# Performance work log

Measured on AMD Instinct MI355X. Metric: run time of the kernel, lower is better.

The kernel has to match this reference:

```python
import jax, jax.numpy as jnp
import numpy as np

LATENT, HIDDEN, OUT = 128, 256, 8
T, B = 32, 16384
LN_EPS = 1e-5
SLOPE = 0.1  # LeakyReLU negative slope


def _leaky(x):
    return jnp.where(x >= 0, x, SLOPE * x)


def _mlp_layer(x, W, b, g, beta):
    # Linear -> LayerNorm -> LeakyReLU(0.1)
    h = x @ W + b
    mu = jnp.mean(h, axis=-1, keepdims=True)
    var = jnp.mean(jnp.square(h - mu), axis=-1, keepdims=True)
    h = (h - mu) * jax.lax.rsqrt(var + LN_EPS) * g + beta
    return _leaky(h)


def setup_inputs() -> dict:
    key = jax.random.key(0)
    ks = jax.random.split(key, 12)
    rn = lambda k, shape, s: jax.random.normal(k, shape, jnp.float32) * s
    z0 = rn(ks[0], (B, LATENT), 1.0)
    # strictly increasing per-sample timestamps [T, B, 1]
    dts = jax.random.uniform(ks[1], (T, B, 1), jnp.float32, 0.01, 0.1)
    ts = jnp.cumsum(dts, axis=0)
    W1 = rn(ks[2], (LATENT + 1, HIDDEN), (LATENT + 1) ** -0.5)
    b1 = jnp.zeros((HIDDEN,), jnp.float32)
    g1 = jnp.ones((HIDDEN,), jnp.float32)
    be1 = jnp.zeros((HIDDEN,), jnp.float32)
    W2 = rn(ks[3], (HIDDEN, LATENT), HIDDEN ** -0.5)
    b2 = jnp.zeros((LATENT,), jnp.float32)
    g2 = jnp.ones((LATENT,), jnp.float32)
    be2 = jnp.zeros((LATENT,), jnp.float32)
    Wl = rn(ks[4], (LATENT, HIDDEN), LATENT ** -0.5)
    bl = jnp.zeros((HIDDEN,), jnp.float32)
    Wo = rn(ks[5], (HIDDEN, OUT), HIDDEN ** -0.5)
    bo = jnp.zeros((OUT,), jnp.float32)
    return dict(z0=z0, ts=ts, W1=W1, b1=b1, g1=g1, be1=be1,
                W2=W2, b2=b2, g2=g2, be2=be2, Wl=Wl, bl=bl, Wo=Wo, bo=bo)


def reference(z0, ts, W1, b1, g1, be1, W2, b2, g2, be2, Wl, bl, Wo, bo):
    def f(z, t):  # MLPODEF: concat time, 2 (Linear->LN->LeakyReLU) layers
        zt = jnp.concatenate([z, t], axis=-1)           # [B, LATENT+1]
        h = _mlp_layer(zt, W1, b1, g1, be1)             # [B, HIDDEN]
        return _mlp_layer(h, W2, b2, g2, be2)           # [B, LATENT]

    t0 = jnp.zeros((1,) + ts.shape[1:], ts.dtype)
    ts_all = jnp.concatenate([t0, ts], axis=0)          # [T+1, B, 1]

    def rk4_step(z, tt):  # one fixed RK4 step per consecutive timestamp pair
        t_cur, t_next = tt                               # [B,1] each
        dt = t_next - t_cur
        k1 = f(z, t_cur)
        k2 = f(z + 0.5 * dt * k1, t_cur + 0.5 * dt)
        k3 = f(z + 0.5 * dt * k2, t_cur + 0.5 * dt)
        k4 = f(z + dt * k3, t_next)
        z_new = z + (dt / 6.0) * (k1 + 2.0 * k2 + 2.0 * k3 + k4)
        return z_new, z_new

    _, zs = jax.lax.scan(rk4_step, z0, (ts_all[:-1], ts_all[1:]))  # [T,B,LATENT] == zs[1:]
    hs = _leaky(zs @ Wl + bl)                            # [T,B,HIDDEN]
    xs = hs @ Wo + bo                                    # [T,B,OUT]
    return xs, zs
```

## Files before the change

kernel.cpp:

```cpp
#include <hip/hip_runtime.h>


#define TSTEPS 32
#define BATCH  16384
#define LAT    128
#define HID    256
#define NOUT   8

using f16x8  = __attribute__((ext_vector_type(8)))  _Float16;
using f16x4  = __attribute__((ext_vector_type(4)))  _Float16;
using f32x16 = __attribute__((ext_vector_type(16))) float;
using f32x4v = __attribute__((ext_vector_type(4)))  float;

#define LO_S 2048.0f
#define LO_I 4.8828125e-4f

__global__ void prep_kernel(const float* __restrict__ W1, const float* __restrict__ b1,
                            const float* __restrict__ g1, const float* __restrict__ be1,
                            const float* __restrict__ W2, const float* __restrict__ b2,
                            const float* __restrict__ g2, const float* __restrict__ be2,
                            const float* __restrict__ Wl,
                            _Float16* __restrict__ w1h, _Float16* __restrict__ w1l,
                            _Float16* __restrict__ w2h, _Float16* __restrict__ w2l,
                            _Float16* __restrict__ wlt,
                            float2* __restrict__ pA, float2* __restrict__ pB,
                            float2* __restrict__ pD, float* __restrict__ b2f)
{
    const int i = blockIdx.x * 256 + threadIdx.x;
    {
        const int h = i >> 7, k = i & 127;
        const float v = W1[k * 256 + h];
        const _Float16 vh = (_Float16)v;
        w1h[i] = vh;
        w1l[i] = (_Float16)((v - (float)vh) * LO_S);
    }
    {
        const int d = i >> 8, h = i & 255;
        const float v = W2[h * 128 + d];
        const _Float16 vh = (_Float16)v;
        w2h[i] = vh;
        w2l[i] = (_Float16)((v - (float)vh) * LO_S);
    }
    {
        const int h = i >> 7, k = i & 127;
        wlt[i] = (_Float16)Wl[k * 256 + h];
    }
    if (i < 256) {
        pA[i] = make_float2(b1[i], W1[128 * 256 + i]);
        pB[i] = make_float2(g1[i], be1[i]);
    }
    if (i < 128) {
        pD[i] = make_float2(g2[i], be2[i]);
        b2f[i] = b2[i];
    }
}

__global__ __launch_bounds__(512, 2) void ode_kernel(
    const float* __restrict__ z0, const float* __restrict__ ts,
    const _Float16* __restrict__ w1hg, const _Float16* __restrict__ w1lg,
    const _Float16* __restrict__ w2hg, const _Float16* __restrict__ w2lg,
    const float2* __restrict__ pAg, const float2* __restrict__ pBg,
    const float2* __restrict__ pDg, const float* __restrict__ b2g,
    float* __restrict__ zs)
{
    __shared__ _Float16 ztH[32 * 128], ztLo[32 * 128];
    __shared__ _Float16 a1H[32 * 256], a1Lo[32 * 256];
    __shared__ float    pt[4096];
    __shared__ float    scrS[8][33], scrQ[8][33];
    __shared__ float2   pA[256], pB[256], pD[128];
    __shared__ float    b2s[128];

    const int tid  = threadIdx.x;
    const int w    = tid >> 6;
    const int l    = tid & 63;
    const int li   = l & 31;
    const int lh   = l >> 5;
    const int samp = li;
    const int t2   = w >> 1;
    const int kh   = w & 1;
    const long gsamp = (long)blockIdx.x * 32 + li;
    char* ztHB = (char*)ztH;  char* ztLB = (char*)ztLo;
    char* a1HB = (char*)a1H;  char* a1LB = (char*)a1Lo;

    if (tid < 256) { pA[tid] = pAg[tid]; pB[tid] = pBg[tid]; }
    if (tid < 128) { pD[tid] = pDg[tid]; b2s[tid] = b2g[tid]; }

    f16x8 w1h[8], w1l[8];
    {
        const int r1 = 32 * w + li;
        #pragma unroll
        for (int kt = 0; kt < 8; ++kt) {
            const int off = r1 * 128 + kt * 16 + lh * 8;
            w1h[kt] = *(const f16x8*)(w1hg + off);
            w1l[kt] = *(const f16x8*)(w1lg + off);
        }
    }
    f16x8 w2h[8], w2l[8];
    {
        const int r2 = 32 * t2 + li;
        #pragma unroll
        for (int kt = 0; kt < 8; ++kt) {
            const int off = r2 * 256 + (8 * kh + kt) * 16 + lh * 8;
            w2h[kt] = *(const f16x8*)(w2hg + off);
            w2l[kt] = *(const f16x8*)(w2lg + off);
        }
    }

    float zor[16], znw[16];
    if (kh == 0) {
        #pragma unroll
        for (int rg = 0; rg < 4; ++rg) {
            const int lat0 = 32 * t2 + 8 * rg + 4 * lh;
            f32x4v v = *(const f32x4v*)(z0 + gsamp * 128 + lat0);
            f16x4 hv, lv;
            #pragma unroll
            for (int j = 0; j < 4; ++j) {
                zor[rg * 4 + j] = v[j];
                hv[j] = (_Float16)v[j];
                lv[j] = (_Float16)((v[j] - (float)hv[j]) * LO_S);
            }
            const int slot = lat0 >> 3;
            const int bo = samp * 256 + ((slot ^ (samp & 15)) << 4) + 8 * lh;
            *(f16x4*)(ztHB + bo) = hv;
            *(f16x4*)(ztLB + bo) = lv;
        }
    }
    __syncthreads();

    #pragma unroll 1
    for (int step = 0; step < TSTEPS; ++step) {
        const float tc = (step == 0) ? 0.f : ts[(long)(step - 1) * BATCH + gsamp];
        const float tn = ts[(long)step * BATCH + gsamp];
        const float dt = tn - tc;
        if (kh == 0) {
            #pragma unroll
            for (int i = 0; i < 16; ++i) znw[i] = zor[i];
        }

        #pragma unroll 1
        for (int stg = 0; stg < 4; ++stg) {
            const float tstg = (stg == 0) ? tc : (stg == 3) ? tn : fmaf(0.5f, dt, tc);
            f32x16 ah = {}, al = {};
            #pragma unroll
            for (int kt = 0; kt < 8; ++kt) {
                const int kc = kt * 2 + lh;
                const int bo = samp * 256 + ((kc ^ (samp & 15)) << 4);
                f16x8 bh = *(const f16x8*)(ztHB + bo);
                f16x8 bl = *(const f16x8*)(ztLB + bo);
                ah = __builtin_amdgcn_mfma_f32_32x32x16_f16(w1h[kt], bh, ah, 0, 0, 0);
                al = __builtin_amdgcn_mfma_f32_32x32x16_f16(w1l[kt], bh, al, 0, 0, 0);
                al = __builtin_amdgcn_mfma_f32_32x32x16_f16(w1h[kt], bl, al, 0, 0, 0);
            }
            float s = 0.f, q = 0.f;
            #pragma unroll
            for (int rg = 0; rg < 4; ++rg) {
                #pragma unroll
                for (int j = 0; j < 4; ++j) {
                    const int hid = 32 * w + 8 * rg + 4 * lh + j;
                    const float2 ab = pA[hid];
                    float h = ah[rg * 4 + j] + LO_I * al[rg * 4 + j] + fmaf(tstg, ab.y, ab.x);
                    ah[rg * 4 + j] = h;
                    s += h; q += h * h;
                }
            }
            s += __shfl_xor(s, 32);
            q += __shfl_xor(q, 32);
            if (l < 32) { scrS[w][samp] = s; scrQ[w][samp] = q; }
            __syncthreads();
            {
                float ssum = 0.f, qsum = 0.f;
                #pragma unroll
                for (int ww = 0; ww < 8; ++ww) { ssum += scrS[ww][samp]; qsum += scrQ[ww][samp]; }
                const float mu = ssum * (1.f / 256.f);
                const float rs = rsqrtf(qsum * (1.f / 256.f) - mu * mu + 1e-5f);
                #pragma unroll
                for (int rg = 0; rg < 4; ++rg) {
                    f16x4 hv, lv;
                    #pragma unroll
                    for (int j = 0; j < 4; ++j) {
                        const int hid = 32 * w + 8 * rg + 4 * lh + j;
                        const float2 gb = pB[hid];
                        float a = fmaf((ah[rg * 4 + j] - mu) * rs, gb.x, gb.y);
                        a = fmaxf(a, 0.1f * a);
                        hv[j] = (_Float16)a;
                        lv[j] = (_Float16)((a - (float)hv[j]) * LO_S);
                    }
                    const int slot = 4 * w + rg;
                    const int bo = samp * 512 + ((slot ^ (samp & 31)) << 4) + 8 * lh;
                    *(f16x4*)(a1HB + bo) = hv;
                    *(f16x4*)(a1LB + bo) = lv;
                }
            }
            __syncthreads();
            f32x16 ch = {}, cl = {};
            #pragma unroll
            for (int kt = 0; kt < 8; ++kt) {
                const int kc = (8 * kh + kt) * 2 + lh;
                const int bo = samp * 512 + ((kc ^ (samp & 31)) << 4);
                f16x8 bh = *(const f16x8*)(a1HB + bo);
                f16x8 bl = *(const f16x8*)(a1LB + bo);
                ch = __builtin_amdgcn_mfma_f32_32x32x16_f16(w2h[kt], bh, ch, 0, 0, 0);
                cl = __builtin_amdgcn_mfma_f32_32x32x16_f16(w2l[kt], bh, cl, 0, 0, 0);
                cl = __builtin_amdgcn_mfma_f32_32x32x16_f16(w2h[kt], bl, cl, 0, 0, 0);
            }
            if (kh == 1) {
                #pragma unroll
                for (int rg = 0; rg < 4; ++rg)
                    #pragma unroll
                    for (int j = 0; j < 4; ++j) {
                        const int row = 8 * rg + 4 * lh + j;
                        pt[(t2 * 32 + row) * 32 + samp] =
                            ch[rg * 4 + j] + LO_I * cl[rg * 4 + j];
                    }
            }
            __syncthreads();
            float h2[16];
            if (kh == 0) {
                float s2 = 0.f, q2 = 0.f;
                #pragma unroll
                for (int rg = 0; rg < 4; ++rg) {
                    #pragma unroll
                    for (int j = 0; j < 4; ++j) {
                        const int row = 8 * rg + 4 * lh + j;
                        const float v = ch[rg * 4 + j] + LO_I * cl[rg * 4 + j]
                                      + pt[(t2 * 32 + row) * 32 + samp]
                                      + b2s[32 * t2 + row];
                        h2[rg * 4 + j] = v;
                        s2 += v; q2 += v * v;
                    }
                }
                s2 += __shfl_xor(s2, 32);
                q2 += __shfl_xor(q2, 32);
                if (l < 32) { scrS[t2][samp] = s2; scrQ[t2][samp] = q2; }
            }
            __syncthreads();
            if (kh == 0) {
                float ssum = 0.f, qsum = 0.f;
                #pragma unroll
                for (int tt = 0; tt < 4; ++tt) { ssum += scrS[tt][samp]; qsum += scrQ[tt][samp]; }
                const float mu2 = ssum * (1.f / 128.f);
                const float rs2 = rsqrtf(qsum * (1.f / 128.f) - mu2 * mu2 + 1e-5f);
                const float c6  = (stg == 1 || stg == 2) ? (1.f / 3.f) : (1.f / 6.f);
                const float cnx = (stg < 2) ? 0.5f : 1.f;
                #pragma unroll
                for (int rg = 0; rg < 4; ++rg) {
                    f16x4 hv, lv;
                    #pragma unroll
                    for (int j = 0; j < 4; ++j) {
                        const int i = rg * 4 + j;
                        const int lat = 32 * t2 + 8 * rg + 4 * lh + j;
                        const float2 gb = pD[lat];
                        float a = fmaf((h2[i] - mu2) * rs2, gb.x, gb.y);
                        a = fmaxf(a, 0.1f * a);
                        znw[i] = fmaf(dt * c6, a, znw[i]);
                        const float za = (stg < 3) ? fmaf(cnx * dt, a, zor[i]) : znw[i];
                        hv[j] = (_Float16)za;
                        lv[j] = (_Float16)((za - (float)hv[j]) * LO_S);
                        if (stg == 3) {
                            pt[lat * 32 + (samp ^ (lat & 31))] = za;
                            zor[i] = za;
                        }
                    }
                    const int slot = 4 * t2 + rg;
                    const int bo = samp * 256 + ((slot ^ (samp & 15)) << 4) + 8 * lh;
                    *(f16x4*)(ztHB + bo) = hv;
                    *(f16x4*)(ztLB + bo) = lv;
                }
            }
            __syncthreads();
        }
        const long zrow = (long)step * BATCH + (long)blockIdx.x * 32;
        for (int ii = tid; ii < 1024; ii += 512) {
            const int sp = ii >> 5, lat0 = (ii & 31) * 4;
            f32x4v v;
            #pragma unroll
            for (int j = 0; j < 4; ++j)
                v[j] = pt[(lat0 + j) * 32 + (sp ^ ((lat0 + j) & 31))];
            *(f32x4v*)(zs + (zrow + sp) * 128 + lat0) = v;
        }
    }
}

__global__ __launch_bounds__(512, 4) void dec_kernel(
    const float* __restrict__ zsin, const _Float16* __restrict__ wlt,
    const float* __restrict__ bl, const float* __restrict__ Wo,
    const float* __restrict__ bo, float* __restrict__ xs)
{
    __shared__ _Float16 zH[32 * 128];
    __shared__ float wo4[256][8];
    __shared__ float bl_s[256];
    __shared__ float scrX[8][32][8];
    __shared__ float bo_s[8];

    const int tid = threadIdx.x;
    const int w = tid >> 6, l = tid & 63, li = l & 31, lh = l >> 5;
    const long r0 = (long)blockIdx.x * 32;
    char* zB = (char*)zH;

    if (tid < 256) bl_s[tid] = bl[tid];
    for (int i = tid; i < 256 * 8; i += 512) wo4[i >> 3][i & 7] = Wo[i];
    if (tid < 8) bo_s[tid] = bo[tid];

    for (int ii = tid; ii < 1024; ii += 512) {
        const int row = ii >> 5, lat0 = (ii & 31) * 4;
        f32x4v v = *(const f32x4v*)(zsin + (r0 + row) * 128 + lat0);
        f16x4 hv;
        #pragma unroll
        for (int j = 0; j < 4; ++j) hv[j] = (_Float16)v[j];
        const int slot = lat0 >> 3;
        *(f16x4*)(zB + row * 256 + ((slot ^ (row & 15)) << 4) + (lat0 & 7) * 2) = hv;
    }

    f16x8 wl8[8];
    #pragma unroll
    for (int kt = 0; kt < 8; ++kt)
        wl8[kt] = *(const f16x8*)(wlt + (32 * w + li) * 128 + kt * 16 + lh * 8);
    __syncthreads();

    f32x16 acc = {};
    #pragma unroll
    for (int kt = 0; kt < 8; ++kt) {
        const int kc = kt * 2 + lh;
        f16x8 b = *(const f16x8*)(zB + li * 256 + ((kc ^ (li & 15)) << 4));
        acc = __builtin_amdgcn_mfma_f32_32x32x16_f16(wl8[kt], b, acc, 0, 0, 0);
    }

    float xo[8];
    #pragma unroll
    for (int o = 0; o < 8; ++o) xo[o] = 0.f;
    #pragma unroll
    for (int rg = 0; rg < 4; ++rg) {
        #pragma unroll
        for (int j = 0; j < 4; ++j) {
            const int hid = 32 * w + 8 * rg + 4 * lh + j;
            float a = acc[rg * 4 + j] + bl_s[hid];
            a = fmaxf(a, 0.1f * a);
            const float4 wa = *(const float4*)&wo4[hid][0];
            const float4 wb = *(const float4*)&wo4[hid][4];
            xo[0] = fmaf(a, wa.x, xo[0]); xo[1] = fmaf(a, wa.y, xo[1]);
            xo[2] = fmaf(a, wa.z, xo[2]); xo[3] = fmaf(a, wa.w, xo[3]);
            xo[4] = fmaf(a, wb.x, xo[4]); xo[5] = fmaf(a, wb.y, xo[5]);
            xo[6] = fmaf(a, wb.z, xo[6]); xo[7] = fmaf(a, wb.w, xo[7]);
        }
    }
    #pragma unroll
    for (int o = 0; o < 8; ++o) xo[o] += __shfl_xor(xo[o], 32);
    if (l < 32) {
        *(float4*)&scrX[w][li][0] = make_float4(xo[0], xo[1], xo[2], xo[3]);
        *(float4*)&scrX[w][li][4] = make_float4(xo[4], xo[5], xo[6], xo[7]);
    }
    __syncthreads();
    if (tid < 256) {
        const int row = tid >> 3, o = tid & 7;
        float s = bo_s[o];
        #pragma unroll
        for (int ww = 0; ww < 8; ++ww) s += scrX[ww][row][o];
        xs[(r0 + row) * 8 + o] = s;
    }
}

extern "C" void kernel_launch(void* const* d_in, const int* in_sizes, int n_in,
                              void* d_out, int out_size, void* d_ws, size_t ws_size,
                              hipStream_t stream) {
    const float* z0  = (const float*)d_in[0];
    const float* ts  = (const float*)d_in[1];
    const float* W1  = (const float*)d_in[2];
    const float* b1  = (const float*)d_in[3];
    const float* g1  = (const float*)d_in[4];
    const float* be1 = (const float*)d_in[5];
    const float* W2  = (const float*)d_in[6];
    const float* b2  = (const float*)d_in[7];
    const float* g2  = (const float*)d_in[8];
    const float* be2 = (const float*)d_in[9];
    const float* Wl  = (const float*)d_in[10];
    const float* bl  = (const float*)d_in[11];
    const float* Wo  = (const float*)d_in[12];
    const float* bo  = (const float*)d_in[13];

    float* xs = (float*)d_out;
    float* zs = (float*)d_out + (size_t)TSTEPS * BATCH * NOUT;

    _Float16* w1h = (_Float16*)d_ws;
    _Float16* w1l = w1h + 32768;
    _Float16* w2h = w1l + 32768;
    _Float16* w2l = w2h + 32768;
    _Float16* wlt = w2l + 32768;
    float2* pA  = (float2*)(wlt + 32768);
    float2* pB  = pA + 256;
    float2* pD  = pB + 256;
    float*  b2f = (float*)(pD + 128);

    prep_kernel<<<dim3(128), dim3(256), 0, stream>>>(
        W1, b1, g1, be1, W2, b2, g2, be2, Wl,
        w1h, w1l, w2h, w2l, wlt, pA, pB, pD, b2f);
    ode_kernel<<<dim3(BATCH / 32), dim3(512), 0, stream>>>(
        z0, ts, w1h, w1l, w2h, w2l, pA, pB, pD, b2f, zs);
    dec_kernel<<<dim3(TSTEPS * BATCH / 32), dim3(512), 0, stream>>>(
        zs, wlt, bl, Wo, bo, xs);
}
```

Baseline: 2.449 ms.

## Stream fragment-ordered weights from global memory and raise occupancy to 4 blocks

Stops holding all split-fp16 W1/W2 MFMA operands in registers (64 f16x8 values per lane). Instead the weights are read from global memory inside each GEMM loop. The prep kernel lays them out in per-wave, per-lane fragment order so each load is a contiguous, coalesced 16-byte read. Launch bounds go from 2 to 4 blocks per CU to use the freed VGPRs for more resident waves. The trade-off is repeated L2/L1 weight traffic and load latency on every RK4 stage, and LDS use per block may limit how much extra occupancy is actually reached.

After: 4.098 ms. 67.4% more time.

```diff
diff --git a/kernel.cpp b/kernel.cpp
--- a/kernel.cpp
+++ b/kernel.cpp
@@ -27,16 +27,23 @@
                             float2* __restrict__ pD, float* __restrict__ b2f)
 {
     const int i = blockIdx.x * 256 + threadIdx.x;
+    const int j    = i & 7;
+    const int lane = (i >> 3) & 63;
+    const int kt   = (i >> 9) & 7;
+    const int wv   = i >> 12;
     {
-        const int h = i >> 7, k = i & 127;
-        const float v = W1[k * 256 + h];
+        const int row = 32 * wv + (lane & 31);
+        const int k   = kt * 16 + 8 * (lane >> 5) + j;
+        const float v = W1[k * 256 + row];
         const _Float16 vh = (_Float16)v;
         w1h[i] = vh;
         w1l[i] = (_Float16)((v - (float)vh) * LO_S);
     }
     {
-        const int d = i >> 8, h = i & 255;
-        const float v = W2[h * 128 + d];
+        const int t2 = wv >> 1, kh = wv & 1;
+        const int row = 32 * t2 + (lane & 31);
+        const int k   = (8 * kh + kt) * 16 + 8 * (lane >> 5) + j;
+        const float v = W2[k * 128 + row];
         const _Float16 vh = (_Float16)v;
         w2h[i] = vh;
         w2l[i] = (_Float16)((v - (float)vh) * LO_S);
@@ -55,7 +62,7 @@
     }
 }
 
-__global__ __launch_bounds__(512, 2) void ode_kernel(
+__global__ __launch_bounds__(512, 4) void ode_kernel(
     const float* __restrict__ z0, const float* __restrict__ ts,
     const _Float16* __restrict__ w1hg, const _Float16* __restrict__ w1lg,
     const _Float16* __restrict__ w2hg, const _Float16* __restrict__ w2lg,
@@ -85,26 +92,11 @@
     if (tid < 256) { pA[tid] = pAg[tid]; pB[tid] = pBg[tid]; }
     if (tid < 128) { pD[tid] = pDg[tid]; b2s[tid] = b2g[tid]; }
 
-    f16x8 w1h[8], w1l[8];
-    {
-        const int r1 = 32 * w + li;
-        #pragma unroll
-        for (int kt = 0; kt < 8; ++kt) {
-            const int off = r1 * 128 + kt * 16 + lh * 8;
-            w1h[kt] = *(const f16x8*)(w1hg + off);
-            w1l[kt] = *(const f16x8*)(w1lg + off);
-        }
-    }
-    f16x8 w2h[8], w2l[8];
-    {
-        const int r2 = 32 * t2 + li;
-        #pragma unroll
-        for (int kt = 0; kt < 8; ++kt) {
-            const int off = r2 * 256 + (8 * kh + kt) * 16 + lh * 8;
-            w2h[kt] = *(const f16x8*)(w2hg + off);
-            w2l[kt] = *(const f16x8*)(w2lg + off);
-        }
-    }
+    const f16x8* w1hv = (const f16x8*)w1hg;
+    const f16x8* w1lv = (const f16x8*)w1lg;
+    const f16x8* w2hv = (const f16x8*)w2hg;
+    const f16x8* w2lv = (const f16x8*)w2lg;
+    const int fbase = w * 8 * 64 + l;
 
     float zor[16], znw[16];
     if (kh == 0) {
@@ -143,13 +135,15 @@
             f32x16 ah = {}, al = {};
             #pragma unroll
             for (int kt = 0; kt < 8; ++kt) {
+                const f16x8 wh = w1hv[fbase + kt * 64];
+                const f16x8 wl = w1lv[fbase + kt * 64];
                 const int kc = kt * 2 + lh;
                 const int bo = samp * 256 + ((kc ^ (samp & 15)) << 4);
                 f16x8 bh = *(const f16x8*)(ztHB + bo);
                 f16x8 bl = *(const f16x8*)(ztLB + bo);
-                ah = __builtin_amdgcn_mfma_f32_32x32x16_f16(w1h[kt], bh, ah, 0, 0, 0);
-                al = __builtin_amdgcn_mfma_f32_32x32x16_f16(w1l[kt], bh, al, 0, 0, 0);
-                al = __builtin_amdgcn_mfma_f32_32x32x16_f16(w1h[kt], bl, al, 0, 0, 0);
+                ah = __builtin_amdgcn_mfma_f32_32x32x16_f16(wh, bh, ah, 0, 0, 0);
+                al = __builtin_amdgcn_mfma_f32_32x32x16_f16(wl, bh, al, 0, 0, 0);
+                al = __builtin_amdgcn_mfma_f32_32x32x16_f16(wh, bl, al, 0, 0, 0);
             }
             float s = 0.f, q = 0.f;
             #pragma unroll
@@ -195,13 +189,15 @@
             f32x16 ch = {}, cl = {};
             #pragma unroll
             for (int kt = 0; kt < 8; ++kt) {
+                const f16x8 wh = w2hv[fbase + kt * 64];
+                const f16x8 wl = w2lv[fbase + kt * 64];
                 const int kc = (8 * kh + kt) * 2 + lh;
                 const int bo = samp * 512 + ((kc ^ (samp & 31)) << 4);
                 f16x8 bh = *(const f16x8*)(a1HB + bo);
                 f16x8 bl = *(const f16x8*)(a1LB + bo);
-                ch = __builtin_amdgcn_mfma_f32_32x32x16_f16(w2h[kt], bh, ch, 0, 0, 0);
-                cl = __builtin_amdgcn_mfma_f32_32x32x16_f16(w2l[kt], bh, cl, 0, 0, 0);
-                cl = __builtin_amdgcn_mfma_f32_32x32x16_f16(w2h[kt], bl, cl, 0, 0, 0);
+                ch = __builtin_amdgcn_mfma_f32_32x32x16_f16(wh, bh, ch, 0, 0, 0);
+                cl = __builtin_amdgcn_mfma_f32_32x32x16_f16(wl, bh, cl, 0, 0, 0);
+                cl = __builtin_amdgcn_mfma_f32_32x32x16_f16(wh, bl, cl, 0, 0, 0);
             }
             if (kh == 1) {
                 #pragma unroll
```
